# Performance work log

Hardware: AMD Instinct MI355X
Metric: run time of the kernel (lower is better)

Reference implementation:

```python
import jax, jax.numpy as jnp
import numpy as np

WS = 7          # window size (square)
HEADS = 16
LOGIT_MAX = float(np.log(1.0 / 0.01))


def _consts():
    # Continuous relative position bias coordinate table, Swin-v2 log-spaced.
    r = np.arange(-(WS - 1), WS)
    table = np.stack(np.meshgrid(r, r, indexing='ij'), axis=-1).astype(np.float32)  # [2W-1, 2W-1, 2]
    table = table / (WS - 1) * 8.0
    table = np.sign(table) * np.log2(np.abs(table) + 1.0) / np.log2(8.0)
    # Relative position index [N, N] into the flattened table.
    coords = np.stack(np.meshgrid(np.arange(WS), np.arange(WS), indexing='ij')).reshape(2, -1)
    rel = coords[:, :, None] - coords[:, None, :]
    idx = (rel[0] + WS - 1) * (2 * WS - 1) + (rel[1] + WS - 1)  # [49, 49]
    return table.reshape(-1, 2), idx.astype(np.int32)


def setup_inputs() -> dict:
    key = jax.random.key(0)
    ks = jax.random.split(key, 6)
    B, N, C = 2048, WS * WS, 512
    d = C // HEADS
    return {
        'x': jax.random.normal(ks[0], (B, N, C), jnp.float32),
        'w_qkv': jax.random.normal(ks[1], (C, 3 * C), jnp.float32) * (C ** -0.5),
        'q_bias': jnp.zeros((C,), jnp.float32),
        'v_bias': jnp.zeros((C,), jnp.float32),
        'logit_scale': jnp.full((HEADS, 1, 1), np.log(10.0), jnp.float32),
        'cpb_w1': jax.random.normal(ks[2], (2, 512), jnp.float32) * (2 ** -0.5),
        'cpb_b1': jnp.zeros((512,), jnp.float32),
        'cpb_w2': jax.random.normal(ks[3], (512, HEADS), jnp.float32) * (512 ** -0.5),
        'proj_w': jax.random.normal(ks[4], (C, C), jnp.float32) * (C ** -0.5),
        'proj_b': jnp.zeros((C,), jnp.float32),
    }


def _l2norm(x):
    # matches tf.math.l2_normalize (eps=1e-12 under a max)
    return x / jnp.sqrt(jnp.maximum(jnp.sum(x * x, axis=-1, keepdims=True), 1e-12))


def reference(x, w_qkv, q_bias, v_bias, logit_scale, cpb_w1, cpb_b1, cpb_w2, proj_w, proj_b):
    table, idx = _consts()
    table = jnp.asarray(table)   # [(2W-1)^2, 2]
    idx = jnp.asarray(idx)       # [N, N] int32 (constant)

    B, N, C = x.shape
    d = C // HEADS

    qkv = (x @ w_qkv).reshape(B, N, 3, HEADS, d).transpose(2, 0, 3, 1, 4)  # [3, B, H, N, d]
    q, k, v = qkv[0], qkv[1], qkv[2]
    q = q + q_bias.reshape(HEADS, 1, d)
    v = v + v_bias.reshape(HEADS, 1, d)

    # cosine attention with clamped learned logit scale
    attn = jnp.einsum('bhnd,bhmd->bhnm', _l2norm(q), _l2norm(k))
    scale = jnp.exp(jnp.minimum(logit_scale, LOGIT_MAX))  # [H,1,1]
    attn = attn * scale[None]

    # CPB MLP -> gather -> sigmoid bias
    bias_table = jax.nn.relu(table @ cpb_w1 + cpb_b1) @ cpb_w2          # [(2W-1)^2, H]
    bias = bias_table[idx.reshape(-1)].reshape(N, N, HEADS).transpose(2, 0, 1)  # [H, N, N]
    bias = 16.0 * jax.nn.sigmoid(bias)

    attn = jax.nn.softmax(attn + bias[None], axis=-1)

    out = jnp.einsum('bhnm,bhmd->bhnd', attn, v).transpose(0, 2, 1, 3).reshape(B, N, C)
    return out @ proj_w + proj_b
```

## Files before the change

kernel.cpp:

```cpp
#include <hip/hip_runtime.h>
#include <hip/hip_bf16.h>

typedef __bf16 bf16;
typedef __attribute__((ext_vector_type(8))) __bf16 bf16x8;
typedef __attribute__((ext_vector_type(4))) __bf16 bf16x4;
typedef __attribute__((ext_vector_type(4))) float floatx4;

#define HEADS 16
#define NTOK 49
#define MROWS (2048 * 49)
#define TILE_E 1568
#define LOGIT_MAX 4.6051702f


__device__ __forceinline__ void gload16(const void* g, void* l) {
  __builtin_amdgcn_global_load_lds((const __attribute__((address_space(1))) void*)g,
                                   (__attribute__((address_space(3))) void*)l, 16, 0, 0);
}

#define BAR() __builtin_amdgcn_s_barrier()
#define WAITDS() asm volatile("s_waitcnt lgkmcnt(0)" ::: "memory")
#define WAITVM(N) asm volatile("s_waitcnt vmcnt(" #N ")" ::: "memory")


__global__ void cvt_x(const float* __restrict__ in, bf16* __restrict__ out, int n4) {
  int i = blockIdx.x * blockDim.x + threadIdx.x;
  const int stride = gridDim.x * blockDim.x;
  for (; i < n4; i += stride) {
    float4 v = ((const float4*)in)[i];
    bf16x4 o;
    o[0] = (bf16)v.x; o[1] = (bf16)v.y; o[2] = (bf16)v.z; o[3] = (bf16)v.w;
    *(bf16x4*)&out[(long)i * 4] = o;
  }
}

__global__ void transpose_bf16(const float* __restrict__ in, bf16* __restrict__ out,
                               int R, int C) {
  int idx = blockIdx.x * blockDim.x + threadIdx.x;
  if (idx < R * C) {
    int r = idx / C, c = idx % C;
    out[(long)c * R + r] = (bf16)in[(long)r * C + c];
  }
}


__global__ void cpb_mlp(const float* __restrict__ w1, const float* __restrict__ b1,
                        const float* __restrict__ w2, float* __restrict__ out169) {
  const int r = blockIdx.x;
  const int ti = r / 13, tj = r % 13;
  float v0 = (float)(ti - 6) * (8.0f / 6.0f);
  float v1 = (float)(tj - 6) * (8.0f / 6.0f);
  float s0 = (v0 > 0.f) ? 1.f : ((v0 < 0.f) ? -1.f : 0.f);
  float s1 = (v1 > 0.f) ? 1.f : ((v1 < 0.f) ? -1.f : 0.f);
  const float t0 = s0 * log2f(fabsf(v0) + 1.0f) * (1.0f / 3.0f);
  const float t1 = s1 * log2f(fabsf(v1) + 1.0f) * (1.0f / 3.0f);

  float acc[16];
#pragma unroll
  for (int h = 0; h < 16; ++h) acc[h] = 0.f;

  for (int c = threadIdx.x; c < 512; c += 64) {
    float hv = fmaxf(t0 * w1[c] + t1 * w1[512 + c] + b1[c], 0.f);
#pragma unroll
    for (int h = 0; h < 16; ++h) acc[h] += hv * w2[c * 16 + h];
  }
#pragma unroll
  for (int h = 0; h < 16; ++h) {
    float s = acc[h];
    for (int off = 32; off > 0; off >>= 1) s += __shfl_down(s, off);
    if (threadIdx.x == 0) out169[r * 16 + h] = s;
  }
}

__global__ void bias_expand(const float* __restrict__ out169, float* __restrict__ bias_sig) {
  int idx = blockIdx.x * blockDim.x + threadIdx.x;
  if (idx < 16 * 64 * 52) {
    int h = idx / 3328;
    int rem = idx % 3328;
    int q = rem / 52, k = rem % 52;
    float val = 0.f;
    if (q < 49 && k < 49) {
      int di = q / 7 - k / 7 + 6;
      int dj = q % 7 - k % 7 + 6;
      float v = out169[(di * 13 + dj) * 16 + h];
      val = 16.0f / (1.0f + expf(-v));
    }
    bias_sig[idx] = val;
  }
}


__device__ __forceinline__ void stage_half(const bf16* __restrict__ G, int ldg,
                                           bf16* lds, int half, int w, int lane) {
#pragma unroll
  for (int j = 0; j < 2; ++j) {
    const int rr = (w * 2 + j) * 8;
    const int row = half * 128 + rr + (lane >> 3);
    const int slot = (lane & 7) ^ (lane >> 3);
    gload16(G + (long)row * ldg + slot * 8, lds + (half * 128 + rr) * 64);
  }
}

#define LOAD_A(MQ, BUF) do { \
  _Pragma("unroll") for (int m_ = 0; m_ < 4; ++m_) \
  _Pragma("unroll") for (int t_ = 0; t_ < 2; ++t_) { \
    const int row_ = wm * 128 + (MQ) * 64 + m_ * 16 + l15; \
    const int s_ = t_ * 4 + g; \
    af[m_][t_] = *(const bf16x8*)&AS[BUF][row_][(s_ ^ (row_ & 7)) * 8]; \
  } } while (0)

#define LOAD_B(NQ, BUF) do { \
  _Pragma("unroll") for (int n_ = 0; n_ < 2; ++n_) \
  _Pragma("unroll") for (int t_ = 0; t_ < 2; ++t_) { \
    const int row_ = wn * 64 + (NQ) * 32 + n_ * 16 + l15; \
    const int s_ = t_ * 4 + g; \
    bfr[NQ][n_][t_] = *(const bf16x8*)&BS[BUF][row_][(s_ ^ (row_ & 7)) * 8]; \
  } } while (0)

#define MFMA_Q(MQ, NQ) do { \
  __builtin_amdgcn_s_setprio(1); \
  _Pragma("unroll") for (int t_ = 0; t_ < 2; ++t_) \
  _Pragma("unroll") for (int m_ = 0; m_ < 4; ++m_) \
  _Pragma("unroll") for (int n_ = 0; n_ < 2; ++n_) \
    acc[(MQ) * 4 + m_][(NQ) * 2 + n_] = __builtin_amdgcn_mfma_f32_16x16x32_bf16( \
        af[m_][t_], bfr[NQ][n_][t_], acc[(MQ) * 4 + m_][(NQ) * 2 + n_], 0, 0, 0); \
  __builtin_amdgcn_s_setprio(0); \
} while (0)

template <int EPI>
__global__ __launch_bounds__(512, 2)
void gemm256(const bf16* __restrict__ A, const bf16* __restrict__ BT,
             void* __restrict__ Cout, const float* __restrict__ bias0,
             const float* __restrict__ bias1,
             bf16* __restrict__ Qp, bf16* __restrict__ Kp, bf16* __restrict__ Vp,
             int NT, int K, long N) {
  __shared__ bf16 AS[2][256][64];
  __shared__ bf16 BS[2][256][64];
  const int tid = threadIdx.x;
  const int lane = tid & 63, w = tid >> 6;
  const int l15 = lane & 15, g = lane >> 4;
  const int wm = w >> 2, wn = w & 3;

  int wg = blockIdx.x;
  wg = (wg & 7) * (gridDim.x >> 3) + (wg >> 3);
  const long m0 = (long)(wg / NT) * 256;
  const long n0 = (long)(wg % NT) * 256;

  const bf16* Ab = A + m0 * K;
  const bf16* Bb = BT + n0 * K;

  floatx4 acc[8][4] = {};
  bf16x8 af[4][2], bfr[2][2][2];

  stage_half(Ab, K, &AS[0][0][0], 0, w, lane);
  stage_half(Ab, K, &AS[0][0][0], 1, w, lane);
  stage_half(Bb, K, &BS[0][0][0], 0, w, lane);
  stage_half(Bb, K, &BS[0][0][0], 1, w, lane);
  stage_half(Bb + 64, K, &BS[1][0][0], 0, w, lane);
  stage_half(Bb + 64, K, &BS[1][0][0], 1, w, lane);
  WAITVM(4);
  BAR();

  const int NI = K >> 7;
  for (int i = 0; i < NI - 1; ++i) {
    const int t1 = 2 * i + 1, t2 = 2 * i + 2, t3 = 2 * i + 3;
    LOAD_A(0, 0); LOAD_B(0, 0);
    stage_half(Ab + t1 * 64, K, &AS[1][0][0], 0, w, lane);
    BAR(); WAITDS(); MFMA_Q(0, 0); BAR();
    LOAD_B(1, 0);
    stage_half(Ab + t1 * 64, K, &AS[1][0][0], 1, w, lane);
    BAR(); WAITDS(); MFMA_Q(0, 1); BAR();
    LOAD_A(1, 0);
    stage_half(Bb + t2 * 64, K, &BS[0][0][0], 0, w, lane);
    BAR(); WAITDS(); MFMA_Q(1, 0); BAR();
    stage_half(Bb + t2 * 64, K, &BS[0][0][0], 1, w, lane);
    WAITVM(4);
    BAR(); MFMA_Q(1, 1); BAR();
    LOAD_A(0, 1); LOAD_B(0, 1);
    stage_half(Ab + t2 * 64, K, &AS[0][0][0], 0, w, lane);
    BAR(); WAITDS(); MFMA_Q(0, 0); BAR();
    LOAD_B(1, 1);
    stage_half(Ab + t2 * 64, K, &AS[0][0][0], 1, w, lane);
    BAR(); WAITDS(); MFMA_Q(0, 1); BAR();
    LOAD_A(1, 1);
    stage_half(Bb + t3 * 64, K, &BS[1][0][0], 0, w, lane);
    BAR(); WAITDS(); MFMA_Q(1, 0); BAR();
    stage_half(Bb + t3 * 64, K, &BS[1][0][0], 1, w, lane);
    WAITVM(4);
    BAR(); MFMA_Q(1, 1); BAR();
  }
  {
    const int t1 = 2 * NI - 1;
    LOAD_A(0, 0); LOAD_B(0, 0);
    stage_half(Ab + t1 * 64, K, &AS[1][0][0], 0, w, lane);
    BAR(); WAITDS(); MFMA_Q(0, 0); BAR();
    LOAD_B(1, 0);
    stage_half(Ab + t1 * 64, K, &AS[1][0][0], 1, w, lane);
    BAR(); WAITDS(); MFMA_Q(0, 1); BAR();
    LOAD_A(1, 0);
    BAR(); WAITDS(); MFMA_Q(1, 0); BAR();
    WAITVM(0);
    BAR(); MFMA_Q(1, 1); BAR();
    LOAD_A(0, 1); LOAD_B(0, 1);
    BAR(); WAITDS(); MFMA_Q(0, 0); BAR();
    LOAD_B(1, 1);
    BAR(); WAITDS(); MFMA_Q(0, 1); BAR();
    LOAD_A(1, 1);
    BAR(); WAITDS(); MFMA_Q(1, 0); BAR();
    WAITDS(); MFMA_Q(1, 1);
  }

  if (EPI == 0) {
    const int mat = (int)(n0 >> 9);
    bf16* const dst = (mat == 0) ? Qp : ((mat == 1) ? Kp : Vp);
    float badd4[4];
    unsigned off4[4];
#pragma unroll
    for (int n = 0; n < 4; ++n) {
      const int coln = (int)n0 + wn * 64 + n * 16;
      const int hh = (coln >> 5) & 15;
      const int d = (coln & 16) + l15;
      off4[n] = (unsigned)hh * TILE_E + d;
      badd4[n] = (mat == 0) ? bias0[coln + l15]
               : ((mat == 2) ? bias1[coln + l15 - 1024] : 0.0f);
    }
#pragma unroll
    for (int m = 0; m < 8; ++m) {
#pragma unroll
      for (int r = 0; r < 4; ++r) {
        const unsigned row = (unsigned)m0 + wm * 128 + m * 16 + g * 4 + r;
        const unsigned b = row / 49u;
        const unsigned nr = row - b * 49u;
        const unsigned ebase = b * (16u * TILE_E) + nr * 32u;
#pragma unroll
        for (int n = 0; n < 4; ++n)
          dst[ebase + off4[n]] = (bf16)(acc[m][n][r] + badd4[n]);
      }
    }
  } else {
#pragma unroll
    for (int m = 0; m < 8; ++m) {
#pragma unroll
      for (int n = 0; n < 4; ++n) {
        const long col = n0 + wn * 64 + n * 16 + l15;
        const float badd = bias0[col];
#pragma unroll
        for (int r = 0; r < 4; ++r) {
          const long row = m0 + wm * 128 + m * 16 + g * 4 + r;
          ((float*)Cout)[row * N + col] = acc[m][n][r] + badd;
        }
      }
    }
  }
}


__global__ __launch_bounds__(256)
void attn_mfma(const bf16* __restrict__ Qa, const bf16* __restrict__ Ka,
               const bf16* __restrict__ Va, const float* __restrict__ bias_sig,
               const float* __restrict__ logit_scale, bf16* __restrict__ aout) {
  __shared__ __align__(16) bf16 Vlds[4][2048];
  const int tid = threadIdx.x;
  const int wave = tid >> 6, lane = tid & 63;
  const int l15 = lane & 15, g = lane >> 4;
  const int bh = blockIdx.x * 4 + wave;
  const int h = bh & 15;
  const long tbase = (long)bh * TILE_E;
  const bf16* Qt = Qa + tbase;
  const bf16* Kt = Ka + tbase;
  const bf16* Vt = Va + tbase;
  bf16* VL = Vlds[wave];

#pragma unroll
  for (int j = 0; j < 4; ++j)
    gload16(Vt + j * 512 + lane * 8, VL + j * 512);

  const float scale = __expf(fminf(logit_scale[h], LOGIT_MAX));

  bf16x8 kf[4];
#pragma unroll
  for (int kt = 0; kt < 4; ++kt) {
    const int row = kt * 16 + l15;
    bf16x8 raw = *(const bf16x8*)(Kt + row * 32 + g * 8);
    float fv[8], ss = 0.f;
#pragma unroll
    for (int j = 0; j < 8; ++j) { fv[j] = (float)raw[j]; ss += fv[j] * fv[j]; }
    ss += __shfl_xor(ss, 16);
    ss += __shfl_xor(ss, 32);
    const float rk = rsqrtf(fmaxf(ss, 1e-12f));
#pragma unroll
    for (int j = 0; j < 8; ++j) kf[kt][j] = (bf16)(fv[j] * rk);
  }

  asm volatile("s_waitcnt vmcnt(0)" ::: "memory");
  __builtin_amdgcn_sched_barrier(0);
  bf16x8 vf[2][2];
#pragma unroll
  for (int dt = 0; dt < 2; ++dt)
#pragma unroll
    for (int t = 0; t < 2; ++t)
#pragma unroll
      for (int i = 0; i < 8; ++i) {
        const int kk = t * 32 + (i >> 2) * 16 + g * 4 + (i & 3);
        vf[dt][t][i] = VL[kk * 32 + dt * 16 + l15];
      }

  const floatx4 zero = {};

  for (int qt = 0; qt < 4; ++qt) {
    const int qrow = qt * 16 + l15;
    bf16x8 qraw = *(const bf16x8*)(Qt + qrow * 32 + g * 8);
    float fq[8], ssq = 0.f;
#pragma unroll
    for (int j = 0; j < 8; ++j) { fq[j] = (float)qraw[j]; ssq += fq[j] * fq[j]; }
    ssq += __shfl_xor(ssq, 16);
    ssq += __shfl_xor(ssq, 32);
    const float rq = rsqrtf(fmaxf(ssq, 1e-12f));
    bf16x8 qf;
#pragma unroll
    for (int j = 0; j < 8; ++j) qf[j] = (bf16)(fq[j] * rq);

    float4 b4[4];
#pragma unroll
    for (int kt = 0; kt < 4; ++kt)
      b4[kt] = *(const float4*)(bias_sig + h * 3328 + qrow * 52 + kt * 16 + g * 4);

    floatx4 st[4];
#pragma unroll
    for (int kt = 0; kt < 4; ++kt)
      st[kt] = __builtin_amdgcn_mfma_f32_16x16x32_bf16(kf[kt], qf, zero, 0, 0, 0);

    float sv[4][4];
    float m = -1e30f;
#pragma unroll
    for (int kt = 0; kt < 4; ++kt)
#pragma unroll
      for (int r = 0; r < 4; ++r) {
        const int k = kt * 16 + g * 4 + r;
        const float s = (k < NTOK) ? st[kt][r] * scale + ((const float*)&b4[kt])[r] : -1e30f;
        sv[kt][r] = s;
        m = fmaxf(m, s);
      }
    m = fmaxf(m, __shfl_xor(m, 16));
    m = fmaxf(m, __shfl_xor(m, 32));
    float l = 0.f;
#pragma unroll
    for (int kt = 0; kt < 4; ++kt)
#pragma unroll
      for (int r = 0; r < 4; ++r) {
        const float p = __expf(sv[kt][r] - m);
        sv[kt][r] = p;
        l += p;
      }
    l += __shfl_xor(l, 16);
    l += __shfl_xor(l, 32);
    const float inv = 1.0f / l;

    bf16x8 pa[2];
#pragma unroll
    for (int t = 0; t < 2; ++t)
#pragma unroll
      for (int i = 0; i < 8; ++i)
        pa[t][i] = (bf16)(sv[2 * t + (i >> 2)][i & 3] * inv);

    floatx4 ot[2] = {};
#pragma unroll
    for (int dt = 0; dt < 2; ++dt)
#pragma unroll
      for (int t = 0; t < 2; ++t)
        ot[dt] = __builtin_amdgcn_mfma_f32_16x16x32_bf16(pa[t], vf[dt][t], ot[dt], 0, 0, 0);

#pragma unroll
    for (int dt = 0; dt < 2; ++dt)
#pragma unroll
      for (int r = 0; r < 4; ++r) {
        const int qg2 = qt * 16 + g * 4 + r;
        if (qg2 < NTOK)
          aout[((long)(bh >> 4) * NTOK + qg2) * 512 + h * 32 + dt * 16 + l15] =
              (bf16)ot[dt][r];
      }
  }
}


extern "C" void kernel_launch(void* const* d_in, const int* in_sizes, int n_in,
                              void* d_out, int out_size, void* d_ws, size_t ws_size,
                              hipStream_t stream) {
  (void)in_sizes; (void)n_in; (void)out_size; (void)ws_size;
  const float* x           = (const float*)d_in[0];
  const float* w_qkv       = (const float*)d_in[1];
  const float* q_bias      = (const float*)d_in[2];
  const float* v_bias      = (const float*)d_in[3];
  const float* logit_scale = (const float*)d_in[4];
  const float* cpb_w1      = (const float*)d_in[5];
  const float* cpb_b1      = (const float*)d_in[6];
  const float* cpb_w2      = (const float*)d_in[7];
  const float* proj_w      = (const float*)d_in[8];
  const float* proj_b      = (const float*)d_in[9];
  float* out = (float*)d_out;

  char* ws = (char*)d_ws;
  const size_t ARR_B  = 102760448;
  const size_t WQT_B  = 1572864;
  const size_t PJT_B  = 524288;
  const size_t T169_B = 10816;
  bf16*  Qa       = (bf16*)ws;
  bf16*  Ka       = (bf16*)(ws + ARR_B);
  bf16*  Va       = (bf16*)(ws + 2 * ARR_B);
  bf16*  xbf      = (bf16*)(ws + 3 * ARR_B);
  bf16*  wqkvT    = (bf16*)(ws + 4 * ARR_B);
  bf16*  projT    = (bf16*)(ws + 4 * ARR_B + WQT_B);
  float* tab169   = (float*)(ws + 4 * ARR_B + WQT_B + PJT_B);
  float* bias_sig = (float*)(ws + 4 * ARR_B + WQT_B + PJT_B + T169_B);

  cvt_x<<<2048, 256, 0, stream>>>(x, xbf, MROWS * 512 / 4);
  transpose_bf16<<<3072, 256, 0, stream>>>(w_qkv, wqkvT, 512, 1536);
  transpose_bf16<<<1024, 256, 0, stream>>>(proj_w, projT, 512, 512);
  cpb_mlp<<<169, 64, 0, stream>>>(cpb_w1, cpb_b1, cpb_w2, tab169);
  bias_expand<<<208, 256, 0, stream>>>(tab169, bias_sig);

  gemm256<0><<<392 * 6, 512, 0, stream>>>(xbf, wqkvT, nullptr, q_bias, v_bias,
                                          Qa, Ka, Va, 6, 512, 1536);
  attn_mfma<<<8192, 256, 0, stream>>>(Qa, Ka, Va, bias_sig, logit_scale, xbf);
  gemm256<1><<<392 * 2, 512, 0, stream>>>(xbf, projT, out, proj_b, nullptr,
                                          nullptr, nullptr, nullptr, 2, 512, 512);
}
```

Baseline: 555.0 us.

## Replace pipelined 256x256 GEMM with simple 128x128 single-buffer GEMM

Replaces the 512-thread 256x256-tile GEMM, which had a hand-scheduled double-buffered LDS pipeline, with a 256-thread 128x128-tile kernel. The new kernel loads one K-tile per iteration between two __syncthreads calls, with no overlap of loads and MFMA. The smaller tile and 4 blocks per CU aim to raise occupancy and grid count for better load balance. The cost is lower data reuse per tile and exposed global-load latency, since there is no software pipelining.

```diff
diff --git a/kernel.cpp b/kernel.cpp
--- a/kernel.cpp
+++ b/kernel.cpp
@@ -17,10 +17,6 @@
   __builtin_amdgcn_global_load_lds((const __attribute__((address_space(1))) void*)g,
                                    (__attribute__((address_space(3))) void*)l, 16, 0, 0);
 }
-
-#define BAR() __builtin_amdgcn_s_barrier()
-#define WAITDS() asm volatile("s_waitcnt lgkmcnt(0)" ::: "memory")
-#define WAITVM(N) asm volatile("s_waitcnt vmcnt(" #N ")" ::: "memory")
 
 
 __global__ void cvt_x(const float* __restrict__ in, bf16* __restrict__ out, int n4) {
@@ -90,124 +86,67 @@
 }
 
 
-__device__ __forceinline__ void stage_half(const bf16* __restrict__ G, int ldg,
-                                           bf16* lds, int half, int w, int lane) {
-#pragma unroll
-  for (int j = 0; j < 2; ++j) {
-    const int rr = (w * 2 + j) * 8;
-    const int row = half * 128 + rr + (lane >> 3);
+__device__ __forceinline__ void stage_tile(const bf16* __restrict__ G, int ldg,
+                                           bf16* lds, int w, int lane) {
+#pragma unroll
+  for (int j = 0; j < 4; ++j) {
+    const int rr = w * 32 + j * 8;
+    const int row = rr + (lane >> 3);
     const int slot = (lane & 7) ^ (lane >> 3);
-    gload16(G + (long)row * ldg + slot * 8, lds + (half * 128 + rr) * 64);
-  }
-}
-
-#define LOAD_A(MQ, BUF) do { \
-  _Pragma("unroll") for (int m_ = 0; m_ < 4; ++m_) \
-  _Pragma("unroll") for (int t_ = 0; t_ < 2; ++t_) { \
-    const int row_ = wm * 128 + (MQ) * 64 + m_ * 16 + l15; \
-    const int s_ = t_ * 4 + g; \
-    af[m_][t_] = *(const bf16x8*)&AS[BUF][row_][(s_ ^ (row_ & 7)) * 8]; \
-  } } while (0)
-
-#define LOAD_B(NQ, BUF) do { \
-  _Pragma("unroll") for (int n_ = 0; n_ < 2; ++n_) \
-  _Pragma("unroll") for (int t_ = 0; t_ < 2; ++t_) { \
-    const int row_ = wn * 64 + (NQ) * 32 + n_ * 16 + l15; \
-    const int s_ = t_ * 4 + g; \
-    bfr[NQ][n_][t_] = *(const bf16x8*)&BS[BUF][row_][(s_ ^ (row_ & 7)) * 8]; \
-  } } while (0)
-
-#define MFMA_Q(MQ, NQ) do { \
-  __builtin_amdgcn_s_setprio(1); \
-  _Pragma("unroll") for (int t_ = 0; t_ < 2; ++t_) \
-  _Pragma("unroll") for (int m_ = 0; m_ < 4; ++m_) \
-  _Pragma("unroll") for (int n_ = 0; n_ < 2; ++n_) \
-    acc[(MQ) * 4 + m_][(NQ) * 2 + n_] = __builtin_amdgcn_mfma_f32_16x16x32_bf16( \
-        af[m_][t_], bfr[NQ][n_][t_], acc[(MQ) * 4 + m_][(NQ) * 2 + n_], 0, 0, 0); \
-  __builtin_amdgcn_s_setprio(0); \
-} while (0)
+    gload16(G + (long)row * ldg + slot * 8, lds + rr * 64);
+  }
+}
 
 template <int EPI>
-__global__ __launch_bounds__(512, 2)
-void gemm256(const bf16* __restrict__ A, const bf16* __restrict__ BT,
+__global__ __launch_bounds__(256, 4)
+void gemm128(const bf16* __restrict__ A, const bf16* __restrict__ BT,
              void* __restrict__ Cout, const float* __restrict__ bias0,
              const float* __restrict__ bias1,
              bf16* __restrict__ Qp, bf16* __restrict__ Kp, bf16* __restrict__ Vp,
              int NT, int K, long N) {
-  __shared__ bf16 AS[2][256][64];
-  __shared__ bf16 BS[2][256][64];
+  __shared__ bf16 AS[128][64];
+  __shared__ bf16 BS[128][64];
   const int tid = threadIdx.x;
   const int lane = tid & 63, w = tid >> 6;
   const int l15 = lane & 15, g = lane >> 4;
-  const int wm = w >> 2, wn = w & 3;
+  const int wm = w >> 1, wn = w & 1;
 
   int wg = blockIdx.x;
-  wg = (wg & 7) * (gridDim.x >> 3) + (wg >> 3);
-  const long m0 = (long)(wg / NT) * 256;
-  const long n0 = (long)(wg % NT) * 256;
+  wg = (wg & 7) * ((int)gridDim.x >> 3) + (wg >> 3);
+  const long m0 = (long)(wg / NT) * 128;
+  const long n0 = (long)(wg % NT) * 128;
 
   const bf16* Ab = A + m0 * K;
   const bf16* Bb = BT + n0 * K;
 
-  floatx4 acc[8][4] = {};
-  bf16x8 af[4][2], bfr[2][2][2];
-
-  stage_half(Ab, K, &AS[0][0][0], 0, w, lane);
-  stage_half(Ab, K, &AS[0][0][0], 1, w, lane);
-  stage_half(Bb, K, &BS[0][0][0], 0, w, lane);
-  stage_half(Bb, K, &BS[0][0][0], 1, w, lane);
-  stage_half(Bb + 64, K, &BS[1][0][0], 0, w, lane);
-  stage_half(Bb + 64, K, &BS[1][0][0], 1, w, lane);
-  WAITVM(4);
-  BAR();
-
-  const int NI = K >> 7;
-  for (int i = 0; i < NI - 1; ++i) {
-    const int t1 = 2 * i + 1, t2 = 2 * i + 2, t3 = 2 * i + 3;
-    LOAD_A(0, 0); LOAD_B(0, 0);
-    stage_half(Ab + t1 * 64, K, &AS[1][0][0], 0, w, lane);
-    BAR(); WAITDS(); MFMA_Q(0, 0); BAR();
-    LOAD_B(1, 0);
-    stage_half(Ab + t1 * 64, K, &AS[1][0][0], 1, w, lane);
-    BAR(); WAITDS(); MFMA_Q(0, 1); BAR();
-    LOAD_A(1, 0);
-    stage_half(Bb + t2 * 64, K, &BS[0][0][0], 0, w, lane);
-    BAR(); WAITDS(); MFMA_Q(1, 0); BAR();
-    stage_half(Bb + t2 * 64, K, &BS[0][0][0], 1, w, lane);
-    WAITVM(4);
-    BAR(); MFMA_Q(1, 1); BAR();
-    LOAD_A(0, 1); LOAD_B(0, 1);
-    stage_half(Ab + t2 * 64, K, &AS[0][0][0], 0, w, lane);
-    BAR(); WAITDS(); MFMA_Q(0, 0); BAR();
-    LOAD_B(1, 1);
-    stage_half(Ab + t2 * 64, K, &AS[0][0][0], 1, w, lane);
-    BAR(); WAITDS(); MFMA_Q(0, 1); BAR();
-    LOAD_A(1, 1);
-    stage_half(Bb + t3 * 64, K, &BS[1][0][0], 0, w, lane);
-    BAR(); WAITDS(); MFMA_Q(1, 0); BAR();
-    stage_half(Bb + t3 * 64, K, &BS[1][0][0], 1, w, lane);
-    WAITVM(4);
-    BAR(); MFMA_Q(1, 1); BAR();
-  }
-  {
-    const int t1 = 2 * NI - 1;
-    LOAD_A(0, 0); LOAD_B(0, 0);
-    stage_half(Ab + t1 * 64, K, &AS[1][0][0], 0, w, lane);
-    BAR(); WAITDS(); MFMA_Q(0, 0); BAR();
-    LOAD_B(1, 0);
-    stage_half(Ab + t1 * 64, K, &AS[1][0][0], 1, w, lane);
-    BAR(); WAITDS(); MFMA_Q(0, 1); BAR();
-    LOAD_A(1, 0);
-    BAR(); WAITDS(); MFMA_Q(1, 0); BAR();
-    WAITVM(0);
-    BAR(); MFMA_Q(1, 1); BAR();
-    LOAD_A(0, 1); LOAD_B(0, 1);
-    BAR(); WAITDS(); MFMA_Q(0, 0); BAR();
-    LOAD_B(1, 1);
-    BAR(); WAITDS(); MFMA_Q(0, 1); BAR();
-    LOAD_A(1, 1);
-    BAR(); WAITDS(); MFMA_Q(1, 0); BAR();
-    WAITDS(); MFMA_Q(1, 1);
+  floatx4 acc[4][4] = {};
+
+  const int NKT = K >> 6;
+  for (int kt = 0; kt < NKT; ++kt) {
+    __syncthreads();
+    stage_tile(Ab + kt * 64, K, &AS[0][0], w, lane);
+    stage_tile(Bb + kt * 64, K, &BS[0][0], w, lane);
+    __syncthreads();
+#pragma unroll
+    for (int t = 0; t < 2; ++t) {
+      const int s = t * 4 + g;
+      bf16x8 af[4], bfr[4];
+#pragma unroll
+      for (int m = 0; m < 4; ++m) {
+        const int row = wm * 64 + m * 16 + l15;
+        af[m] = *(const bf16x8*)&AS[row][(s ^ (row & 7)) * 8];
+      }
+#pragma unroll
+      for (int n = 0; n < 4; ++n) {
+        const int row = wn * 64 + n * 16 + l15;
+        bfr[n] = *(const bf16x8*)&BS[row][(s ^ (row & 7)) * 8];
+      }
+#pragma unroll
+      for (int m = 0; m < 4; ++m)
+#pragma unroll
+        for (int n = 0; n < 4; ++n)
+          acc[m][n] = __builtin_amdgcn_mfma_f32_16x16x32_bf16(af[m], bfr[n], acc[m][n], 0, 0, 0);
+    }
   }
 
   if (EPI == 0) {
@@ -225,10 +164,10 @@
                : ((mat == 2) ? bias1[coln + l15 - 1024] : 0.0f);
     }
 #pragma unroll
-    for (int m = 0; m < 8; ++m) {
+    for (int m = 0; m < 4; ++m) {
 #pragma unroll
       for (int r = 0; r < 4; ++r) {
-        const unsigned row = (unsigned)m0 + wm * 128 + m * 16 + g * 4 + r;
+        const unsigned row = (unsigned)m0 + wm * 64 + m * 16 + g * 4 + r;
         const unsigned b = row / 49u;
         const unsigned nr = row - b * 49u;
         const unsigned ebase = b * (16u * TILE_E) + nr * 32u;
@@ -239,14 +178,14 @@
     }
   } else {
 #pragma unroll
-    for (int m = 0; m < 8; ++m) {
+    for (int m = 0; m < 4; ++m) {
 #pragma unroll
       for (int n = 0; n < 4; ++n) {
         const long col = n0 + wn * 64 + n * 16 + l15;
         const float badd = bias0[col];
 #pragma unroll
         for (int r = 0; r < 4; ++r) {
-          const long row = m0 + wm * 128 + m * 16 + g * 4 + r;
+          const long row = m0 + wm * 64 + m * 16 + g * 4 + r;
           ((float*)Cout)[row * N + col] = acc[m][n][r] + badd;
         }
       }
@@ -419,9 +358,9 @@
   cpb_mlp<<<169, 64, 0, stream>>>(cpb_w1, cpb_b1, cpb_w2, tab169);
   bias_expand<<<208, 256, 0, stream>>>(tab169, bias_sig);
 
-  gemm256<0><<<392 * 6, 512, 0, stream>>>(xbf, wqkvT, nullptr, q_bias, v_bias,
-                                          Qa, Ka, Va, 6, 512, 1536);
+  gemm128<0><<<784 * 12, 256, 0, stream>>>(xbf, wqkvT, nullptr, q_bias, v_bias,
+                                           Qa, Ka, Va, 12, 512, 1536);
   attn_mfma<<<8192, 256, 0, stream>>>(Qa, Ka, Va, bias_sig, logit_scale, xbf);
-  gemm256<1><<<392 * 2, 512, 0, stream>>>(xbf, projT, out, proj_b, nullptr,
-                                          nullptr, nullptr, nullptr, 2, 512, 512);
-}
+  gemm128<1><<<784 * 4, 256, 0, stream>>>(xbf, projT, out, proj_b, nullptr,
+                                          nullptr, nullptr, nullptr, 4, 512, 512);
+}
```

Result: faster. 501.2 us (-9.7%).
